# Performance work log

Measured on AMD Instinct MI355X. Metric: run time of the kernel, lower is better.

## Reference

```python
import jax, jax.numpy as jnp
import numpy as np


def _embedding_distances(dictionary, x_flat):
    # dictionary: [D, C], x_flat: [T, C] -> [T, D]
    dict_norms = jnp.sum(dictionary * dictionary, axis=-1)          # [D]
    x_norms = jnp.sum(x_flat * x_flat, axis=-1)                     # [T]
    dots = jnp.einsum('tc,dc->td', x_flat, dictionary)              # [T, D]
    return -2.0 * dots + dict_norms[None, :] + x_norms[:, None]


def _quantize(x, dictionary):
    # x: [N, C, H, W]
    N, C, H, W = x.shape
    cl = jnp.transpose(x, (0, 2, 3, 1))                             # [N, H, W, C]
    diffs = _embedding_distances(dictionary, cl.reshape(-1, C))     # [NHW, D]
    idxs = jnp.argmin(diffs, axis=-1).reshape(N, H, W)              # [N, H, W]
    embedded = jnp.transpose(dictionary[idxs], (0, 3, 1, 2))        # [N, C, H, W]
    embedded_pt = jax.lax.stop_gradient(embedded) + (x - jax.lax.stop_gradient(x))
    return embedded, embedded_pt, idxs


def setup_inputs() -> dict:
    key = jax.random.key(0)
    k1, k2, k3 = jax.random.split(key, 3)
    N, C, H, W, D = 32, 256, 32, 32, 1024
    return {
        'inputs': jax.random.normal(k1, (N, C, H, W), dtype=jnp.float32),
        'inputs_thermal': jax.random.normal(k2, (N, C, H, W), dtype=jnp.float32),
        'dictionary': jax.random.normal(k3, (D, C), dtype=jnp.float32),
    }


def reference(inputs, inputs_thermal, dictionary):
    embedded, embedded_pt, idxs = _quantize(inputs, dictionary)
    embedded_t, embedded_pt_t, idxs_t = _quantize(inputs_thermal, dictionary)
    return (embedded, embedded_pt, idxs, embedded_t, embedded_pt_t, idxs_t)
```

## Files before the change

kernel.cpp:

```cpp
#include <hip/hip_runtime.h>

#define NB    32
#define CCH   256
#define HW    1024
#define NPIX  (NB*HW)
#define DDICT 1024

#define EMB_ELEMS  ((size_t)NB*CCH*HW)
#define SEC_ELEMS  (2*EMB_ELEMS + NPIX)

#define TPX  128
#define TD   128
#define NDT  (DDICT/TD)
#define BK   32
#define NKC  (CCH/BK)
#define NPH  (NDT*NKC)

#define TAU  0.05f

#define RB   8

typedef __attribute__((ext_vector_type(8))) short bf16x8;
typedef __attribute__((ext_vector_type(4))) float f32x4;

__device__ inline ushort split_rne(float f, float& rest) {
    uint u = __float_as_uint(f);
    uint r = u + 0x7FFFu + ((u >> 16) & 1u);
    rest = f - __uint_as_float(r & 0xFFFF0000u);
    return (ushort)(r >> 16);
}

__device__ inline ushort rne_bf16(float f) {
    uint u = __float_as_uint(f);
    return (ushort)((u + 0x7FFFu + ((u >> 16) & 1u)) >> 16);
}

__device__ inline void gll16(const void* g, void* l) {
    __builtin_amdgcn_global_load_lds(
        (const __attribute__((address_space(1))) uint*)g,
        (__attribute__((address_space(3))) uint*)l,
        16, 0, 0);
}

__global__ void dict_prep_kernel(const float* __restrict__ dict,
                                 ushort* __restrict__ dHs,
                                 ushort* __restrict__ dMs,
                                 float* __restrict__ dictT,
                                 float* __restrict__ norms) {
    int d = blockIdx.x;
    int lane = threadIdx.x;
    float4 f = ((const float4*)(dict + (size_t)d * CCH))[lane];
    float v[4] = {f.x, f.y, f.z, f.w};
    ushort h[4], m[4];
#pragma unroll
    for (int i = 0; i < 4; ++i) {
        float r1;
        h[i] = split_rne(v[i], r1);
        m[i] = rne_bf16(r1);
    }
    int c0 = lane * 4;
    int kc = c0 >> 5, oct = (c0 >> 3) & 3, e0 = c0 & 7;
    int dt = d >> 7, dd = d & 127;
    int slot = (oct + (dd >> 1)) & 3;
    size_t base = ((size_t)(dt * NKC + kc)) * 4096 + dd * 32 + slot * 8 + e0;
    *(ushort4*)(dHs + base) = make_ushort4(h[0], h[1], h[2], h[3]);
    *(ushort4*)(dMs + base) = make_ushort4(m[0], m[1], m[2], m[3]);
#pragma unroll
    for (int j = 0; j < 4; ++j)
        dictT[(size_t)(c0 + j) * DDICT + d] = v[j];

    if (lane == 0) {
        const float4* row = (const float4*)(dict + (size_t)d * CCH);
        float s = 0.f;
#pragma unroll 8
        for (int i = 0; i < CCH / 4; ++i) {
            float4 w = row[i];
            s += w.x * w.x + w.y * w.y + w.z * w.z + w.w * w.w;
        }
        norms[d] = s;
    }
}

__global__ __launch_bounds__(512, 4)
void vq_mega_kernel(const float* __restrict__ x0,
                    const float* __restrict__ x1,
                    const ushort* __restrict__ dHs,
                    const ushort* __restrict__ dMs,
                    const float* __restrict__ norms,
                    const float* __restrict__ dict,
                    const float* __restrict__ dictT,
                    float* __restrict__ out) {
    __shared__ ushort Bs[2][2][4096];
    __shared__ float nrm_s[DDICT];
    __shared__ int   idx_s[TPX];
    __shared__ int   fl_list[TPX];
    __shared__ int   fl_cnt;
    __shared__ float rd_s[8][RB];
    __shared__ int   ri_s[8][RB];
    __shared__ int   bi_s[RB];

    const int t    = threadIdx.x;
    const int lane = t & 63;
    const int wv   = t >> 6;
    const int lx   = lane & 15;
    const int q    = lane >> 4;
    const int m0w  = wv * 16;
    const int z    = blockIdx.y;

    const int g0  = blockIdx.x * TPX;
    const int n   = g0 / HW;
    const int hw0 = g0 % HW;

    const float* x = z ? x1 : x0;
    float* out_base = out + (size_t)z * SEC_ELEMS;
    float* out_emb    = out_base;
    float* out_emb_pt = out_base + EMB_ELEMS;
    float* out_idx    = out_base + 2 * EMB_ELEMS;

    if (t == 0) fl_cnt = 0;
    *(float2*)(nrm_s + t * 2) = *(const float2*)(norms + t * 2);

    const float* xbase = x + (size_t)n * CCH * HW + hw0 + m0w + lx;
    bf16x8 Ah[8], Am[8];
#pragma unroll
    for (int kc = 0; kc < NKC; ++kc) {
        float a_f[8];
#pragma unroll
        for (int j = 0; j < 8; ++j)
            a_f[j] = xbase[(size_t)(kc * BK + q * 8 + j) * HW];
#pragma unroll
        for (int j = 0; j < 8; ++j) {
            float r1;
            ushort h = split_rne(a_f[j], r1);
            Ah[kc][j] = (short)h;
            Am[kc][j] = (short)rne_bf16(r1);
        }
    }

    auto stage = [&](int p, int b) {
#pragma unroll
        for (int plane = 0; plane < 2; ++plane) {
            const ushort* sp = (plane ? dMs : dHs) + (size_t)p * 4096;
            gll16(sp + t * 8, &Bs[b][plane][wv * 512]);
        }
    };

    __syncthreads();
    stage(0, 0);

    float b1r[4], b2r[4]; int i1r[4];
#pragma unroll
    for (int r = 0; r < 4; ++r) {
        b1r[r] = 3.0e38f; b2r[r] = 3.0e38f; i1r[r] = 0;
    }

    for (int dt = 0; dt < NDT; ++dt) {
        f32x4 acc[8] = {};
#pragma unroll
        for (int kc = 0; kc < NKC; ++kc) {
            const int p = dt * 8 + kc;
            asm volatile("s_waitcnt vmcnt(0)" ::: "memory");
            __builtin_amdgcn_s_barrier();
            if (p + 1 < NPH) stage(p + 1, (p + 1) & 1);

            const ushort* bb = &Bs[p & 1][0][0];
            __builtin_amdgcn_s_setprio(1);
#pragma unroll
            for (int ni = 0; ni < 8; ++ni) {
                int nn   = ni * 16 + lx;
                int slot = (q + (nn >> 1)) & 3;
                int off  = nn * 32 + slot * 8;
                bf16x8 Bh = *(const bf16x8*)(bb + off);
                bf16x8 Bm = *(const bf16x8*)(bb + 4096 + off);
                f32x4 c = acc[ni];
                c = __builtin_amdgcn_mfma_f32_16x16x32_bf16(Ah[kc], Bh, c, 0, 0, 0);
                c = __builtin_amdgcn_mfma_f32_16x16x32_bf16(Ah[kc], Bm, c, 0, 0, 0);
                c = __builtin_amdgcn_mfma_f32_16x16x32_bf16(Am[kc], Bh, c, 0, 0, 0);
                acc[ni] = c;
            }
            __builtin_amdgcn_s_setprio(0);
        }

        const int d0 = dt * TD;
        float nrm[8];
#pragma unroll
        for (int ni = 0; ni < 8; ++ni) nrm[ni] = nrm_s[d0 + ni * 16 + lx];

#pragma unroll
        for (int r = 0; r < 4; ++r) {
            float c1 = 3.0e38f, c2 = 3.0e38f; int ci = 0;
#pragma unroll
            for (int ni = 0; ni < 8; ++ni) {
                float dist = fmaf(-2.f, acc[ni][r], nrm[ni]);
                if (dist < c1)      { c2 = c1; c1 = dist; ci = ni * 16 + lx; }
                else if (dist < c2) { c2 = dist; }
            }
#pragma unroll
            for (int off = 1; off < 16; off <<= 1) {
                float o1 = __shfl_xor(c1, off);
                int   oi = __shfl_xor(ci, off);
                float o2 = __shfl_xor(c2, off);
                if (o1 < c1 || (o1 == c1 && oi < ci)) {
                    c2 = fminf(c1, o2); c1 = o1; ci = oi;
                } else {
                    c2 = fminf(c2, o1);
                }
            }
            if (c1 < b1r[r]) {
                b2r[r] = fminf(b1r[r], c2);
                b1r[r] = c1;
                i1r[r] = d0 + ci;
            } else {
                b2r[r] = fminf(b2r[r], c1);
            }
        }
    }

#pragma unroll
    for (int r = 0; r < 4; ++r) {
        if (lx == 0) {
            int loc = m0w + q * 4 + r;
            idx_s[loc] = i1r[r];
            out_idx[g0 + loc] = (float)i1r[r];
            if (b2r[r] - b1r[r] < TAU) {
                int s = atomicAdd(&fl_cnt, 1);
                fl_list[s] = loc;
            }
        }
    }
    __syncthreads();

    {
        const int pg = t & 31;
        const int cg = t >> 5;
        const int hwp = hw0 + pg * 4;
        const float* r0 = dict + (size_t)idx_s[pg * 4 + 0] * CCH;
        const float* r1 = dict + (size_t)idx_s[pg * 4 + 1] * CCH;
        const float* r2 = dict + (size_t)idx_s[pg * 4 + 2] * CCH;
        const float* r3 = dict + (size_t)idx_s[pg * 4 + 3] * CCH;
        const size_t obase = (size_t)n * CCH * HW + hwp;
#pragma unroll
        for (int cq = 0; cq < 4; ++cq) {
            int c = cg * 16 + cq * 4;
            float4 q0 = *(const float4*)(r0 + c);
            float4 q1 = *(const float4*)(r1 + c);
            float4 q2 = *(const float4*)(r2 + c);
            float4 q3 = *(const float4*)(r3 + c);
            float4 v0 = make_float4(q0.x, q1.x, q2.x, q3.x);
            float4 v1 = make_float4(q0.y, q1.y, q2.y, q3.y);
            float4 v2 = make_float4(q0.z, q1.z, q2.z, q3.z);
            float4 v3 = make_float4(q0.w, q1.w, q2.w, q3.w);
            *(float4*)(out_emb    + obase + (size_t)(c + 0) * HW) = v0;
            *(float4*)(out_emb_pt + obase + (size_t)(c + 0) * HW) = v0;
            *(float4*)(out_emb    + obase + (size_t)(c + 1) * HW) = v1;
            *(float4*)(out_emb_pt + obase + (size_t)(c + 1) * HW) = v1;
            *(float4*)(out_emb    + obase + (size_t)(c + 2) * HW) = v2;
            *(float4*)(out_emb_pt + obase + (size_t)(c + 2) * HW) = v2;
            *(float4*)(out_emb    + obase + (size_t)(c + 3) * HW) = v3;
            *(float4*)(out_emb_pt + obase + (size_t)(c + 3) * HW) = v3;
        }
    }

    const int nf = fl_cnt;
    if (nf > 0) {
        float (*xr_)[CCH] = (float(*)[CCH])(&Bs[0][0][0]);
        for (int f0 = 0; f0 < nf; f0 += RB) {
            const int np = min(RB, nf - f0);
            __syncthreads();
            {
                const int p  = t >> 6;
                const int pi = f0 + ((p < np) ? p : (np - 1));
                const int g  = g0 + fl_list[pi];
                const int hw = g % HW;
                const float* xb = x + (size_t)n * CCH * HW + hw;
                const int c0 = (t & 63) * 4;
#pragma unroll
                for (int j = 0; j < 4; ++j)
                    xr_[p][c0 + j] = xb[(size_t)(c0 + j) * HW];
            }
            __syncthreads();

            float ac[2][RB] = {};
            for (int k = 0; k < CCH; ++k) {
                float xp[RB];
#pragma unroll
                for (int p = 0; p < RB; ++p) xp[p] = xr_[p][k];
#pragma unroll
                for (int dd = 0; dd < 2; ++dd) {
                    float v = dictT[(size_t)k * DDICT + dd * 512 + t];
#pragma unroll
                    for (int p = 0; p < RB; ++p)
                        ac[dd][p] = fmaf(xp[p], v, ac[dd][p]);
                }
            }
#pragma unroll
            for (int p = 0; p < RB; ++p) {
                float bd = 3.0e38f; int bi = 0;
#pragma unroll
                for (int dd = 0; dd < 2; ++dd) {
                    int d = dd * 512 + t;
                    float dist = fmaf(-2.f, ac[dd][p], nrm_s[d]);
                    if (dist < bd) { bd = dist; bi = d; }
                }
#pragma unroll
                for (int off = 1; off < 64; off <<= 1) {
                    float od = __shfl_xor(bd, off);
                    int   oi = __shfl_xor(bi, off);
                    if (od < bd || (od == bd && oi < bi)) { bd = od; bi = oi; }
                }
                if (lane == 0) { rd_s[wv][p] = bd; ri_s[wv][p] = bi; }
            }
            __syncthreads();
            if (t < RB) {
                float fb = rd_s[0][t]; int fi = ri_s[0][t];
#pragma unroll
                for (int w2 = 1; w2 < 8; ++w2)
                    if (rd_s[w2][t] < fb ||
                        (rd_s[w2][t] == fb && ri_s[w2][t] < fi)) {
                        fb = rd_s[w2][t]; fi = ri_s[w2][t];
                    }
                bi_s[t] = fi;
                if (t < np) out_idx[g0 + fl_list[f0 + t]] = (float)fi;
            }
            __syncthreads();
            if (t < 256) {
                for (int p = 0; p < np; ++p) {
                    const int g  = g0 + fl_list[f0 + p];
                    const int hw = g % HW;
                    float v = dict[(size_t)bi_s[p] * CCH + t];
                    size_t o = (size_t)n * CCH * HW + (size_t)t * HW + hw;
                    out_emb[o]    = v;
                    out_emb_pt[o] = v;
                }
            }
        }
    }
}

extern "C" void kernel_launch(void* const* d_in, const int* in_sizes, int n_in,
                              void* d_out, int out_size, void* d_ws, size_t ws_size,
                              hipStream_t stream) {
    const float* x0   = (const float*)d_in[0];
    const float* x1   = (const float*)d_in[1];
    const float* dict = (const float*)d_in[2];
    float* out = (float*)d_out;

    float*  norms = (float*)d_ws;
    ushort* dHs   = (ushort*)(norms + DDICT);
    ushort* dMs   = dHs + (size_t)DDICT * CCH;
    float*  dictT = (float*)(dMs + (size_t)DDICT * CCH);

    dict_prep_kernel<<<dim3(DDICT), dim3(64), 0, stream>>>(dict, dHs, dMs,
                                                           dictT, norms);

    vq_mega_kernel<<<dim3(NPIX / TPX, 2), dim3(512), 0, stream>>>(
        x0, x1, dHs, dMs, norms, dict, dictT, out);
}
```

Before: 347.9 us.

## Track top-3 candidates and resolve two-way ties with cheap fp32 pair check

The MFMA epilogue now tracks the best, second and third distances plus the second-best index. Pixels whose top-two gap is ambiguous but third is clear are resolved per wavefront by two exact fp32 dot products, instead of going through the full 1024-entry fp32 rescan. Only pixels with three near-tied candidates use the full fallback. This adds register pressure and shuffle work to the hot reduction loop in exchange for fewer expensive fallback rescans.

```diff
diff --git a/kernel.cpp b/kernel.cpp
--- a/kernel.cpp
+++ b/kernel.cpp
@@ -93,8 +93,10 @@
     __shared__ ushort Bs[2][2][4096];
     __shared__ float nrm_s[DDICT];
     __shared__ int   idx_s[TPX];
-    __shared__ int   fl_list[TPX];
-    __shared__ int   fl_cnt;
+    __shared__ int   fs_list[TPX];
+    __shared__ int   pl_loc[TPX];
+    __shared__ int   pl_i2[TPX];
+    __shared__ int   fs_cnt, pl_cnt;
     __shared__ float rd_s[8][RB];
     __shared__ int   ri_s[8][RB];
     __shared__ int   bi_s[RB];
@@ -117,7 +119,7 @@
     float* out_emb_pt = out_base + EMB_ELEMS;
     float* out_idx    = out_base + 2 * EMB_ELEMS;
 
-    if (t == 0) fl_cnt = 0;
+    if (t == 0) { fs_cnt = 0; pl_cnt = 0; }
     *(float2*)(nrm_s + t * 2) = *(const float2*)(norms + t * 2);
 
     const float* xbase = x + (size_t)n * CCH * HW + hw0 + m0w + lx;
@@ -148,10 +150,11 @@
     __syncthreads();
     stage(0, 0);
 
-    float b1r[4], b2r[4]; int i1r[4];
+    float b1r[4], b2r[4], b3r[4]; int i1r[4], i2r[4];
 #pragma unroll
     for (int r = 0; r < 4; ++r) {
-        b1r[r] = 3.0e38f; b2r[r] = 3.0e38f; i1r[r] = 0;
+        b1r[r] = 3.0e38f; b2r[r] = 3.0e38f; b3r[r] = 3.0e38f;
+        i1r[r] = 0; i2r[r] = 0;
     }
 
     for (int dt = 0; dt < NDT; ++dt) {
@@ -188,30 +191,45 @@
 
 #pragma unroll
         for (int r = 0; r < 4; ++r) {
-            float c1 = 3.0e38f, c2 = 3.0e38f; int ci = 0;
+            float c1 = 3.0e38f, c2 = 3.0e38f, c3 = 3.0e38f;
+            int ci = 0, ci2 = 0;
 #pragma unroll
             for (int ni = 0; ni < 8; ++ni) {
                 float dist = fmaf(-2.f, acc[ni][r], nrm[ni]);
-                if (dist < c1)      { c2 = c1; c1 = dist; ci = ni * 16 + lx; }
-                else if (dist < c2) { c2 = dist; }
+                if (dist < c1) {
+                    c3 = c2; c2 = c1; ci2 = ci; c1 = dist; ci = ni * 16 + lx;
+                } else if (dist < c2) {
+                    c3 = c2; c2 = dist; ci2 = ni * 16 + lx;
+                } else if (dist < c3) {
+                    c3 = dist;
+                }
             }
 #pragma unroll
             for (int off = 1; off < 16; off <<= 1) {
                 float o1 = __shfl_xor(c1, off);
                 int   oi = __shfl_xor(ci, off);
                 float o2 = __shfl_xor(c2, off);
+                int   oi2 = __shfl_xor(ci2, off);
+                float o3 = __shfl_xor(c3, off);
                 if (o1 < c1 || (o1 == c1 && oi < ci)) {
-                    c2 = fminf(c1, o2); c1 = o1; ci = oi;
+                    float n2; int n2i; float n3;
+                    if (c1 < o2) { n2 = c1; n2i = ci;  n3 = fminf(c2, o2); }
+                    else         { n2 = o2; n2i = oi2; n3 = fminf(c1, o3); }
+                    c1 = o1; ci = oi; c2 = n2; ci2 = n2i; c3 = n3;
                 } else {
-                    c2 = fminf(c2, o1);
+                    if (o1 < c2) { c3 = fminf(c2, o2); c2 = o1; ci2 = oi; }
+                    else         { c3 = fminf(c3, o1); }
                 }
             }
             if (c1 < b1r[r]) {
-                b2r[r] = fminf(b1r[r], c2);
-                b1r[r] = c1;
-                i1r[r] = d0 + ci;
+                float n2; int n2i; float n3;
+                if (b1r[r] < c2) { n2 = b1r[r]; n2i = i1r[r];   n3 = fminf(b2r[r], c2); }
+                else             { n2 = c2;     n2i = d0 + ci2; n3 = fminf(b1r[r], c3); }
+                b1r[r] = c1; i1r[r] = d0 + ci;
+                b2r[r] = n2; i2r[r] = n2i; b3r[r] = n3;
             } else {
-                b2r[r] = fminf(b2r[r], c1);
+                if (c1 < b2r[r]) { b3r[r] = fminf(b2r[r], c2); b2r[r] = c1; i2r[r] = d0 + ci; }
+                else             { b3r[r] = fminf(b3r[r], c1); }
             }
         }
     }
@@ -222,9 +240,12 @@
             int loc = m0w + q * 4 + r;
             idx_s[loc] = i1r[r];
             out_idx[g0 + loc] = (float)i1r[r];
-            if (b2r[r] - b1r[r] < TAU) {
-                int s = atomicAdd(&fl_cnt, 1);
-                fl_list[s] = loc;
+            if (b3r[r] - b1r[r] < TAU) {
+                int s = atomicAdd(&fs_cnt, 1);
+                fs_list[s] = loc;
+            } else if (b2r[r] - b1r[r] < TAU) {
+                int s = atomicAdd(&pl_cnt, 1);
+                pl_loc[s] = loc; pl_i2[s] = i2r[r];
             }
         }
     }
@@ -261,7 +282,43 @@
         }
     }
 
-    const int nf = fl_cnt;
+    {
+        float* xw = (float*)&Bs[0][0][0] + wv * CCH;
+        const int npair = pl_cnt;
+        for (int pi = wv; pi < npair; pi += 8) {
+            const int loc = pl_loc[pi];
+            const int j1  = idx_s[loc];
+            const int j2  = pl_i2[pi];
+            const int g   = g0 + loc;
+            const int hw  = g % HW;
+            const float* xb = x + (size_t)n * CCH * HW + hw;
+            for (int k = lane; k < CCH; k += 64) xw[k] = xb[(size_t)k * HW];
+            asm volatile("s_waitcnt lgkmcnt(0)" ::: "memory");
+
+            float dot1 = 0.f, dot2 = 0.f;
+            const float* r1p = dict + (size_t)j1 * CCH;
+            const float* r2p = dict + (size_t)j2 * CCH;
+#pragma unroll 8
+            for (int k = 0; k < CCH; ++k) {
+                float xv = xw[k];
+                dot1 = fmaf(xv, r1p[k], dot1);
+                dot2 = fmaf(xv, r2p[k], dot2);
+            }
+            float d1 = fmaf(-2.f, dot1, nrm_s[j1]);
+            float d2 = fmaf(-2.f, dot2, nrm_s[j2]);
+            if (d2 < d1 || (d2 == d1 && j2 < j1)) {
+                if (lane == 0) out_idx[g] = (float)j2;
+                for (int k = lane; k < CCH; k += 64) {
+                    float v = r2p[k];
+                    size_t o = (size_t)n * CCH * HW + (size_t)k * HW + hw;
+                    out_emb[o]    = v;
+                    out_emb_pt[o] = v;
+                }
+            }
+        }
+    }
+
+    const int nf = fs_cnt;
     if (nf > 0) {
         float (*xr_)[CCH] = (float(*)[CCH])(&Bs[0][0][0]);
         for (int f0 = 0; f0 < nf; f0 += RB) {
@@ -270,7 +327,7 @@
             {
                 const int p  = t >> 6;
                 const int pi = f0 + ((p < np) ? p : (np - 1));
-                const int g  = g0 + fl_list[pi];
+                const int g  = g0 + fs_list[pi];
                 const int hw = g % HW;
                 const float* xb = x + (size_t)n * CCH * HW + hw;
                 const int c0 = (t & 63) * 4;
@@ -320,12 +377,12 @@
                         fb = rd_s[w2][t]; fi = ri_s[w2][t];
                     }
                 bi_s[t] = fi;
-                if (t < np) out_idx[g0 + fl_list[f0 + t]] = (float)fi;
+                if (t < np) out_idx[g0 + fs_list[f0 + t]] = (float)fi;
             }
             __syncthreads();
             if (t < 256) {
                 for (int p = 0; p < np; ++p) {
-                    const int g  = g0 + fl_list[f0 + p];
+                    const int g  = g0 + fs_list[f0 + p];
                     const int hw = g % HW;
                     float v = dict[(size_t)bi_s[p] * CCH + t];
                     size_t o = (size_t)n * CCH * HW + (size_t)t * HW + hw;
```

After: 362.0 us. +4.0%, slower.

## Retile waves to 2x4 MFMA tiles splitting dictionary columns, merge argmin via LDS

Applied to the files above, without the earlier changes.

Changes the per-wave work split from 16 pixels by 128 codes to 32 pixels by 64 codes. Each wave now holds two A fragments and reuses each B fragment loaded from LDS for two MFMA row tiles, which halves the LDS B reads per MFMA. The two code halves produce partial top-2 results that are merged through new shared arrays with an extra barrier. The cost is more A registers, which could limit occupancy under the 512x4 launch bound, plus a small added merge step.

```diff
diff --git a/kernel.cpp b/kernel.cpp
--- a/kernel.cpp
+++ b/kernel.cpp
@@ -95,6 +95,9 @@
     __shared__ int   idx_s[TPX];
     __shared__ int   fl_list[TPX];
     __shared__ int   fl_cnt;
+    __shared__ float mg_b1[2][TPX];
+    __shared__ float mg_b2[2][TPX];
+    __shared__ int   mg_i1[2][TPX];
     __shared__ float rd_s[8][RB];
     __shared__ int   ri_s[8][RB];
     __shared__ int   bi_s[RB];
@@ -102,9 +105,11 @@
     const int t    = threadIdx.x;
     const int lane = t & 63;
     const int wv   = t >> 6;
+    const int h    = wv >> 2;
+    const int pg   = wv & 3;
     const int lx   = lane & 15;
     const int q    = lane >> 4;
-    const int m0w  = wv * 16;
+    const int m0w  = pg * 32;
     const int z    = blockIdx.y;
 
     const int g0  = blockIdx.x * TPX;
@@ -121,20 +126,24 @@
     *(float2*)(nrm_s + t * 2) = *(const float2*)(norms + t * 2);
 
     const float* xbase = x + (size_t)n * CCH * HW + hw0 + m0w + lx;
-    bf16x8 Ah[8], Am[8];
+    bf16x8 Ah[8][2], Am[8][2];
 #pragma unroll
     for (int kc = 0; kc < NKC; ++kc) {
-        float a_f[8];
-#pragma unroll
-        for (int j = 0; j < 8; ++j)
-            a_f[j] = xbase[(size_t)(kc * BK + q * 8 + j) * HW];
-#pragma unroll
-        for (int j = 0; j < 8; ++j) {
-            float r1;
-            ushort h = split_rne(a_f[j], r1);
-            Ah[kc][j] = (short)h;
-            Am[kc][j] = (short)rne_bf16(r1);
-        }
+        float a_f[2][8];
+#pragma unroll
+        for (int mi = 0; mi < 2; ++mi)
+#pragma unroll
+            for (int j = 0; j < 8; ++j)
+                a_f[mi][j] = xbase[(size_t)(kc * BK + q * 8 + j) * HW + mi * 16];
+#pragma unroll
+        for (int mi = 0; mi < 2; ++mi)
+#pragma unroll
+            for (int j = 0; j < 8; ++j) {
+                float r1;
+                ushort hh = split_rne(a_f[mi][j], r1);
+                Ah[kc][mi][j] = (short)hh;
+                Am[kc][mi][j] = (short)rne_bf16(r1);
+            }
     }
 
     auto stage = [&](int p, int b) {
@@ -148,14 +157,16 @@
     __syncthreads();
     stage(0, 0);
 
-    float b1r[4], b2r[4]; int i1r[4];
-#pragma unroll
-    for (int r = 0; r < 4; ++r) {
-        b1r[r] = 3.0e38f; b2r[r] = 3.0e38f; i1r[r] = 0;
-    }
+    float b1r[2][4], b2r[2][4]; int i1r[2][4];
+#pragma unroll
+    for (int mi = 0; mi < 2; ++mi)
+#pragma unroll
+        for (int r = 0; r < 4; ++r) {
+            b1r[mi][r] = 3.0e38f; b2r[mi][r] = 3.0e38f; i1r[mi][r] = 0;
+        }
 
     for (int dt = 0; dt < NDT; ++dt) {
-        f32x4 acc[8] = {};
+        f32x4 acc[2][4] = {};
 #pragma unroll
         for (int kc = 0; kc < NKC; ++kc) {
             const int p = dt * 8 + kc;
@@ -166,78 +177,100 @@
             const ushort* bb = &Bs[p & 1][0][0];
             __builtin_amdgcn_s_setprio(1);
 #pragma unroll
-            for (int ni = 0; ni < 8; ++ni) {
-                int nn   = ni * 16 + lx;
+            for (int ni = 0; ni < 4; ++ni) {
+                int nn   = h * 64 + ni * 16 + lx;
                 int slot = (q + (nn >> 1)) & 3;
                 int off  = nn * 32 + slot * 8;
                 bf16x8 Bh = *(const bf16x8*)(bb + off);
                 bf16x8 Bm = *(const bf16x8*)(bb + 4096 + off);
-                f32x4 c = acc[ni];
-                c = __builtin_amdgcn_mfma_f32_16x16x32_bf16(Ah[kc], Bh, c, 0, 0, 0);
-                c = __builtin_amdgcn_mfma_f32_16x16x32_bf16(Ah[kc], Bm, c, 0, 0, 0);
-                c = __builtin_amdgcn_mfma_f32_16x16x32_bf16(Am[kc], Bh, c, 0, 0, 0);
-                acc[ni] = c;
+#pragma unroll
+                for (int mi = 0; mi < 2; ++mi) {
+                    f32x4 c = acc[mi][ni];
+                    c = __builtin_amdgcn_mfma_f32_16x16x32_bf16(Ah[kc][mi], Bh, c, 0, 0, 0);
+                    c = __builtin_amdgcn_mfma_f32_16x16x32_bf16(Ah[kc][mi], Bm, c, 0, 0, 0);
+                    c = __builtin_amdgcn_mfma_f32_16x16x32_bf16(Am[kc][mi], Bh, c, 0, 0, 0);
+                    acc[mi][ni] = c;
+                }
             }
             __builtin_amdgcn_s_setprio(0);
         }
 
-        const int d0 = dt * TD;
-        float nrm[8];
-#pragma unroll
-        for (int ni = 0; ni < 8; ++ni) nrm[ni] = nrm_s[d0 + ni * 16 + lx];
-
+        const int d0 = dt * TD + h * 64;
+        float nrm[4];
+#pragma unroll
+        for (int ni = 0; ni < 4; ++ni) nrm[ni] = nrm_s[d0 + ni * 16 + lx];
+
+#pragma unroll
+        for (int mi = 0; mi < 2; ++mi)
+#pragma unroll
+            for (int r = 0; r < 4; ++r) {
+                float c1 = 3.0e38f, c2 = 3.0e38f; int ci = 0;
+#pragma unroll
+                for (int ni = 0; ni < 4; ++ni) {
+                    float dist = fmaf(-2.f, acc[mi][ni][r], nrm[ni]);
+                    if (dist < c1)      { c2 = c1; c1 = dist; ci = ni * 16 + lx; }
+                    else if (dist < c2) { c2 = dist; }
+                }
+#pragma unroll
+                for (int off = 1; off < 16; off <<= 1) {
+                    float o1 = __shfl_xor(c1, off);
+                    int   oi = __shfl_xor(ci, off);
+                    float o2 = __shfl_xor(c2, off);
+                    if (o1 < c1 || (o1 == c1 && oi < ci)) {
+                        c2 = fminf(c1, o2); c1 = o1; ci = oi;
+                    } else {
+                        c2 = fminf(c2, o1);
+                    }
+                }
+                if (c1 < b1r[mi][r]) {
+                    b2r[mi][r] = fminf(b1r[mi][r], c2);
+                    b1r[mi][r] = c1;
+                    i1r[mi][r] = d0 + ci;
+                } else {
+                    b2r[mi][r] = fminf(b2r[mi][r], c1);
+                }
+            }
+    }
+
+#pragma unroll
+    for (int mi = 0; mi < 2; ++mi)
 #pragma unroll
         for (int r = 0; r < 4; ++r) {
-            float c1 = 3.0e38f, c2 = 3.0e38f; int ci = 0;
-#pragma unroll
-            for (int ni = 0; ni < 8; ++ni) {
-                float dist = fmaf(-2.f, acc[ni][r], nrm[ni]);
-                if (dist < c1)      { c2 = c1; c1 = dist; ci = ni * 16 + lx; }
-                else if (dist < c2) { c2 = dist; }
-            }
-#pragma unroll
-            for (int off = 1; off < 16; off <<= 1) {
-                float o1 = __shfl_xor(c1, off);
-                int   oi = __shfl_xor(ci, off);
-                float o2 = __shfl_xor(c2, off);
-                if (o1 < c1 || (o1 == c1 && oi < ci)) {
-                    c2 = fminf(c1, o2); c1 = o1; ci = oi;
-                } else {
-                    c2 = fminf(c2, o1);
-                }
-            }
-            if (c1 < b1r[r]) {
-                b2r[r] = fminf(b1r[r], c2);
-                b1r[r] = c1;
-                i1r[r] = d0 + ci;
-            } else {
-                b2r[r] = fminf(b2r[r], c1);
-            }
-        }
-    }
-
-#pragma unroll
-    for (int r = 0; r < 4; ++r) {
-        if (lx == 0) {
-            int loc = m0w + q * 4 + r;
-            idx_s[loc] = i1r[r];
-            out_idx[g0 + loc] = (float)i1r[r];
-            if (b2r[r] - b1r[r] < TAU) {
-                int s = atomicAdd(&fl_cnt, 1);
-                fl_list[s] = loc;
-            }
-        }
-    }
+            if (lx == 0) {
+                int row = m0w + mi * 16 + q * 4 + r;
+                mg_b1[h][row] = b1r[mi][r];
+                mg_i1[h][row] = i1r[mi][r];
+                mg_b2[h][row] = b2r[mi][r];
+            }
+        }
     __syncthreads();
 
+    if (t < TPX) {
+        float b1a = mg_b1[0][t]; int i1a = mg_i1[0][t]; float b2a = mg_b2[0][t];
+        float b1b = mg_b1[1][t]; int i1b = mg_i1[1][t]; float b2b = mg_b2[1][t];
+        float b1, b2; int i1;
+        if (b1b < b1a || (b1b == b1a && i1b < i1a)) {
+            b1 = b1b; i1 = i1b; b2 = fminf(b2b, b1a);
+        } else {
+            b1 = b1a; i1 = i1a; b2 = fminf(b2a, b1b);
+        }
+        idx_s[t] = i1;
+        out_idx[g0 + t] = (float)i1;
+        if (b2 - b1 < TAU) {
+            int s = atomicAdd(&fl_cnt, 1);
+            fl_list[s] = t;
+        }
+    }
+    __syncthreads();
+
     {
-        const int pg = t & 31;
-        const int cg = t >> 5;
-        const int hwp = hw0 + pg * 4;
-        const float* r0 = dict + (size_t)idx_s[pg * 4 + 0] * CCH;
-        const float* r1 = dict + (size_t)idx_s[pg * 4 + 1] * CCH;
-        const float* r2 = dict + (size_t)idx_s[pg * 4 + 2] * CCH;
-        const float* r3 = dict + (size_t)idx_s[pg * 4 + 3] * CCH;
+        const int pg2 = t & 31;
+        const int cg  = t >> 5;
+        const int hwp = hw0 + pg2 * 4;
+        const float* r0 = dict + (size_t)idx_s[pg2 * 4 + 0] * CCH;
+        const float* r1 = dict + (size_t)idx_s[pg2 * 4 + 1] * CCH;
+        const float* r2 = dict + (size_t)idx_s[pg2 * 4 + 2] * CCH;
+        const float* r3 = dict + (size_t)idx_s[pg2 * 4 + 3] * CCH;
         const size_t obase = (size_t)n * CCH * HW + hwp;
 #pragma unroll
         for (int cq = 0; cq < 4; ++cq) {
```

Result: slower. 539.3 us (+55.0%).
